# Kernel tuning notes

Hardware: AMD Instinct MI355X
Metric: run time of the kernel (lower is better)

## Reference

```python
import jax, jax.numpy as jnp
import numpy as np

PE_DIM = 40  # pe_dim; gaussian PE scale factor = pe_dim // 2


def _batched_linear(x, wb):
    # x: [B, N, D], wb: [B, D+1, H] (last row is bias)
    return jnp.einsum('bnd,bdh->bnh', x, wb[:, :-1, :]) + wb[:, -1:, :]


def setup_inputs() -> dict:
    key = jax.random.key(0)
    ks = jax.random.split(key, 8)
    B, N = 16, 16384
    H = 256
    pe_out = 3 * PE_DIM  # 120
    s = 0.05  # keep ReLU-chain activations bounded
    return {
        'x': jax.random.normal(ks[0], (B, N, 3), dtype=jnp.float32),
        'wb0': jax.random.normal(ks[1], (B, pe_out + 1, H), dtype=jnp.float32) * s,
        'wb1': jax.random.normal(ks[2], (B, H + 1, H), dtype=jnp.float32) * s,
        'wb2': jax.random.normal(ks[3], (B, H + 1, H), dtype=jnp.float32) * s,
        'wb3': jax.random.normal(ks[4], (B, H + 1, H), dtype=jnp.float32) * s,
        'wb4': jax.random.normal(ks[5], (B, H + 1, H), dtype=jnp.float32) * s,
        'wb_out': jax.random.normal(ks[6], (B, H + 1, 1), dtype=jnp.float32) * s,
        'rand_freqs': jax.random.normal(ks[7], (3 * (PE_DIM // 2), 3), dtype=jnp.float32),  # feat_sigma=1
    }


def reference(x, wb0, wb1, wb2, wb3, wb4, wb_out, rand_freqs):
    # Gaussian positional encoding: k = x . (rand_freqs * pe_dim//2)
    k = jnp.einsum('bnd,fd->bnf', x, rand_freqs * (PE_DIM // 2))  # [B,N,60]
    h = jnp.concatenate([jnp.sin(k), jnp.cos(k)], axis=-1)        # [B,N,120]
    for wb in (wb0, wb1, wb2, wb3, wb4):
        h = jax.nn.relu(_batched_linear(h, wb))
    out = _batched_linear(h, wb_out)  # [B,N,1]
    return out
```

## Files before the change

### kernel.cpp

```cpp
#include <hip/hip_runtime.h>
#include <hip/hip_bf16.h>


#define H 256
#define MT 64
#define PE_NF 60

typedef __attribute__((ext_vector_type(8))) short s16x8;
typedef __attribute__((ext_vector_type(4))) float f32x4;

static __device__ __forceinline__ unsigned short f2bf(float v) {
  unsigned int u = __float_as_uint(v);
  return (unsigned short)((u + 0x7FFFu + ((u >> 16) & 1u)) >> 16);
}
static __device__ __forceinline__ float bf2f(unsigned short u) {
  return __uint_as_float(((unsigned int)u) << 16);
}
static __device__ __forceinline__ int hswz(int row, int chunk) {
  return (chunk & ~7) | ((chunk ^ row) & 7);
}

static __device__ __forceinline__ void bar_raw() {
  asm volatile("s_barrier" ::: "memory");
}
static __device__ __forceinline__ void bar_lgkm() {
  asm volatile("s_waitcnt lgkmcnt(0)\n\ts_barrier" ::: "memory");
}

__global__ __launch_bounds__(256) void prep_weights(
    const float* __restrict__ wb0, const float* __restrict__ wb1,
    const float* __restrict__ wb2, const float* __restrict__ wb3,
    const float* __restrict__ wb4,
    unsigned short* __restrict__ w0p, unsigned short* __restrict__ w14p,
    float* __restrict__ biases) {
  int z = blockIdx.z;
  int li = z >> 4, b = z & 15;
  int k0 = blockIdx.x * 32;
  int n0 = blockIdx.y * 32;
  int Ks;
  const float* src;
  unsigned short* dst;
  if (li == 0) {
    Ks = 120;
    if (k0 >= 128) return;
    src = wb0 + (size_t)b * 121 * H;
    dst = w0p + (size_t)b * 32768;
  } else {
    Ks = 256;
    const float* srcs[4] = {wb1, wb2, wb3, wb4};
    src = srcs[li - 1] + (size_t)b * 257 * H;
    dst = w14p + ((size_t)(li - 1) * 16 + b) * 65536;
  }
  __shared__ float tile[32][33];
  int t = threadIdx.x;
  int tx = t & 31, ty = t >> 5;
#pragma unroll
  for (int i = 0; i < 4; ++i) {
    int k = k0 + ty + i * 8;
    tile[ty + i * 8][tx] = (k < Ks) ? src[(size_t)k * H + n0 + tx] : 0.f;
  }
  if (k0 == 0 && ty == 0)
    biases[((size_t)li * 16 + b) * H + n0 + tx] = src[(size_t)Ks * H + n0 + tx];
  __syncthreads();
  if (t < 128) {
    int nn = t & 31, kg = t >> 5;
    int n = n0 + nn;
    int kt = k0 >> 5;
    union { unsigned short us[8]; s16x8 v; } pk;
#pragma unroll
    for (int j = 0; j < 8; ++j) pk.us[j] = f2bf(tile[kg * 8 + j][nn]);
    *(s16x8*)&dst[(size_t)(kt * 16 + (n >> 4)) * 512 + (kg * 16 + (n & 15)) * 8] = pk.v;
  }
}

template <int NKT, bool LAST>
static __device__ __forceinline__ void mlp_layer(
    const unsigned short* __restrict__ wl, const unsigned short* __restrict__ wln,
    const float* __restrict__ bl, unsigned short* __restrict__ h_s,
    const int rlane, const int kgrp, const int wc, const int l,
    s16x8 (&wf)[2][4]) {
  static_assert((NKT & 1) == 0, "ping-pong parity needs even NKT");
  f32x4 acc[4][4];
#pragma unroll
  for (int ct = 0; ct < 4; ++ct) {
    f32x4 bini = *(const f32x4*)(bl + wc * 64 + ct * 16 + kgrp * 4);
#pragma unroll
    for (int rt = 0; rt < 4; ++rt) acc[rt][ct] = bini;
  }

  const unsigned short* fp = wl + (size_t)(wc * 4) * 512 + l * 8;

  s16x8 af[2][4];
  {
    const int cs = hswz(rlane, kgrp) * 8;
#pragma unroll
    for (int rt = 0; rt < 4; ++rt)
      af[0][rt] = *(const s16x8*)&h_s[(rt * 16 + rlane) * 256 + cs];
  }

#pragma unroll
  for (int kt = 0; kt < NKT; ++kt) {
    if (kt + 1 < NKT) {
#pragma unroll
      for (int c = 0; c < 4; ++c)
        wf[(kt + 1) & 1][c] = *(const s16x8*)(fp + ((kt + 1) * 16 + c) * 512);
      const int cs = hswz(rlane, (kt + 1) * 4 + kgrp) * 8;
#pragma unroll
      for (int rt = 0; rt < 4; ++rt)
        af[(kt + 1) & 1][rt] = *(const s16x8*)&h_s[(rt * 16 + rlane) * 256 + cs];
    } else if (!LAST) {
      const unsigned short* fpn = wln + (size_t)(wc * 4) * 512 + l * 8;
#pragma unroll
      for (int c = 0; c < 4; ++c)
        wf[0][c] = *(const s16x8*)(fpn + c * 512);
    }
    __builtin_amdgcn_s_setprio(1);
#pragma unroll
    for (int rt = 0; rt < 4; ++rt)
#pragma unroll
      for (int ct = 0; ct < 4; ++ct)
        acc[rt][ct] = __builtin_amdgcn_mfma_f32_16x16x32_bf16(
            wf[kt & 1][ct], af[kt & 1][rt], acc[rt][ct], 0, 0, 0);
    __builtin_amdgcn_s_setprio(0);
  }
  bar_raw();

  const int sub = (kgrp & 1) * 4;
  const int cbase = wc * 8 + (kgrp >> 1);
#pragma unroll
  for (int rt = 0; rt < 4; ++rt) {
    const int m = rt * 16 + rlane;
    const int rowb = m * 256;
#pragma unroll
    for (int ct = 0; ct < 4; ++ct) {
      const int cs = hswz(m, cbase + ct * 2);
      float v0 = fmaxf(acc[rt][ct][0], 0.f);
      float v1 = fmaxf(acc[rt][ct][1], 0.f);
      float v2 = fmaxf(acc[rt][ct][2], 0.f);
      float v3 = fmaxf(acc[rt][ct][3], 0.f);
      union { __hip_bfloat162 h2[2]; uint2 u; } pk;
      pk.h2[0] = __float22bfloat162_rn(float2{v0, v1});
      pk.h2[1] = __float22bfloat162_rn(float2{v2, v3});
      *(uint2*)&h_s[rowb + cs * 8 + sub] = pk.u;
    }
  }
  bar_lgkm();
}

__global__ __launch_bounds__(256, 3) void hyponerf_main(
    const float* __restrict__ x, const float* __restrict__ rfreq,
    const float* __restrict__ wbout,
    const unsigned short* __restrict__ w0p, const unsigned short* __restrict__ w14p,
    const float* __restrict__ biases, float* __restrict__ out) {
  __shared__ __align__(16) unsigned short h_s[MT * 256];
  __shared__ float fr_s[PE_NF * 3];
  __shared__ float x_s[MT * 3];
  __shared__ float wout_s[H + 1];

  int bid = blockIdx.x;
  int logical = (bid & 7) * 512 + (bid >> 3);
  int b  = logical >> 8;
  int mt = logical & 255;

  int t = threadIdx.x;
  int wc = t >> 6, l = t & 63;
  int rlane = l & 15;
  int kgrp  = l >> 4;

  const unsigned short* wl0 = w0p + (size_t)b * 32768;
  const unsigned short* wl1 = w14p + (size_t)(0 * 16 + b) * 65536;
  const unsigned short* wl2 = w14p + (size_t)(1 * 16 + b) * 65536;
  const unsigned short* wl3 = w14p + (size_t)(2 * 16 + b) * 65536;
  const unsigned short* wl4 = w14p + (size_t)(3 * 16 + b) * 65536;

  s16x8 wf[2][4];
  {
    const unsigned short* fp0 = wl0 + (size_t)(wc * 4) * 512 + l * 8;
#pragma unroll
    for (int c = 0; c < 4; ++c) wf[0][c] = *(const s16x8*)(fp0 + c * 512);
  }

  const float* xg = x + ((size_t)b * 16384 + (size_t)mt * MT) * 3;
  for (int i = t; i < MT * 3; i += 256) x_s[i] = xg[i];
  for (int i = t; i < PE_NF * 3; i += 256) fr_s[i] = rfreq[i] * 20.0f;
  for (int i = t; i < H + 1; i += 256) wout_s[i] = wbout[(size_t)b * (H + 1) + i];
  bar_lgkm();

  {
    int r = t >> 2;
    int q = t & 3;
    float x0 = x_s[r * 3 + 0], x1 = x_s[r * 3 + 1], x2 = x_s[r * 3 + 2];
    int rowb = r * 256;
#pragma unroll
    for (int cc = 0; cc < 4; ++cc) {
      int ch = q * 4 + cc;
      union { unsigned short us[8]; s16x8 v; } pk;
#pragma unroll
      for (int j = 0; j < 8; ++j) {
        int n = ch * 8 + j;
        float v = 0.f;
        if (n < 60) {
          float kv = x0 * fr_s[n * 3] + x1 * fr_s[n * 3 + 1] + x2 * fr_s[n * 3 + 2];
          v = __sinf(kv);
        } else if (n < 120) {
          int f = n - 60;
          float kv = x0 * fr_s[f * 3] + x1 * fr_s[f * 3 + 1] + x2 * fr_s[f * 3 + 2];
          v = __cosf(kv);
        }
        pk.us[j] = f2bf(v);
      }
      *(s16x8*)&h_s[rowb + hswz(r, ch) * 8] = pk.v;
    }
  }
  bar_lgkm();

  mlp_layer<4, false>(wl0, wl1, biases + (size_t)(0 * 16 + b) * H, h_s,
                      rlane, kgrp, wc, l, wf);
  mlp_layer<8, false>(wl1, wl2, biases + (size_t)(1 * 16 + b) * H, h_s,
                      rlane, kgrp, wc, l, wf);
  mlp_layer<8, false>(wl2, wl3, biases + (size_t)(2 * 16 + b) * H, h_s,
                      rlane, kgrp, wc, l, wf);
  mlp_layer<8, false>(wl3, wl4, biases + (size_t)(3 * 16 + b) * H, h_s,
                      rlane, kgrp, wc, l, wf);
  mlp_layer<8, true >(wl4, wl4, biases + (size_t)(4 * 16 + b) * H, h_s,
                      rlane, kgrp, wc, l, wf);

  {
    int r = t >> 2;
    int q = t & 3;
    int rowb = r * 256;
    float sum = 0.f;
#pragma unroll
    for (int c = 0; c < 8; ++c) {
      int ch = q * 8 + c;
      const s16x8 hv = *(const s16x8*)&h_s[rowb + hswz(r, ch) * 8];
#pragma unroll
      for (int j = 0; j < 8; ++j)
        sum += bf2f((unsigned short)hv[j]) * wout_s[ch * 8 + j];
    }
    sum += __shfl_xor(sum, 1);
    sum += __shfl_xor(sum, 2);
    if (q == 0)
      out[(size_t)b * 16384 + (size_t)mt * MT + r] = sum + wout_s[H];
  }
}

extern "C" void kernel_launch(void* const* d_in, const int* in_sizes, int n_in,
                              void* d_out, int out_size, void* d_ws, size_t ws_size,
                              hipStream_t stream) {
  const float* x     = (const float*)d_in[0];
  const float* wb0   = (const float*)d_in[1];
  const float* wb1   = (const float*)d_in[2];
  const float* wb2   = (const float*)d_in[3];
  const float* wb3   = (const float*)d_in[4];
  const float* wb4   = (const float*)d_in[5];
  const float* wbout = (const float*)d_in[6];
  const float* rfreq = (const float*)d_in[7];
  float* out = (float*)d_out;

  char* ws = (char*)d_ws;
  unsigned short* w0p  = (unsigned short*)ws;
  unsigned short* w14p = (unsigned short*)(ws + (size_t)16 * 32768 * 2);
  float* biases = (float*)(ws + (size_t)16 * 32768 * 2
                              + (size_t)64 * 65536 * 2);

  prep_weights<<<dim3(8, 8, 80), 256, 0, stream>>>(wb0, wb1, wb2, wb3, wb4,
                                                   w0p, w14p, biases);
  hyponerf_main<<<dim3(4096), 256, 0, stream>>>(x, rfreq, wbout, w0p, w14p,
                                                biases, out);
}
```

Baseline: 170.9 us.

## Fuse output projection into last layer epilogue and simplify address arithmetic

The final 256->1 projection is now computed straight from the last layer's fp32 accumulators in registers. Each wave reduces across lanes with shuffles and writes partial sums to a small shared buffer, which replaces the bf16 write-back to shared memory, a barrier and the re-read of h_s. Weight and activation addresses now use precomputed byte pointers and base offsets to cut per-iteration index math. The output projection also consumes unrounded fp32 activations instead of bf16, and the cached output weights add 16 registers per thread, which may pressure occupancy.

```diff
diff --git a/kernel.cpp b/kernel.cpp
--- a/kernel.cpp
+++ b/kernel.cpp
@@ -12,9 +12,6 @@
 static __device__ __forceinline__ unsigned short f2bf(float v) {
   unsigned int u = __float_as_uint(v);
   return (unsigned short)((u + 0x7FFFu + ((u >> 16) & 1u)) >> 16);
-}
-static __device__ __forceinline__ float bf2f(unsigned short u) {
-  return __uint_as_float(((unsigned int)u) << 16);
 }
 static __device__ __forceinline__ int hswz(int row, int chunk) {
   return (chunk & ~7) | ((chunk ^ row) & 7);
@@ -75,10 +72,10 @@
 
 template <int NKT, bool LAST>
 static __device__ __forceinline__ void mlp_layer(
-    const unsigned short* __restrict__ wl, const unsigned short* __restrict__ wln,
-    const float* __restrict__ bl, unsigned short* __restrict__ h_s,
+    const char* fpb, const char* fpn, const float* __restrict__ bl,
+    unsigned short* __restrict__ h_s,
     const int rlane, const int kgrp, const int wc, const int l,
-    s16x8 (&wf)[2][4]) {
+    s16x8 (&wf)[2][4], const float* wout_r, float* psum) {
   static_assert((NKT & 1) == 0, "ping-pong parity needs even NKT");
   f32x4 acc[4][4];
 #pragma unroll
@@ -88,31 +85,31 @@
     for (int rt = 0; rt < 4; ++rt) acc[rt][ct] = bini;
   }
 
-  const unsigned short* fp = wl + (size_t)(wc * 4) * 512 + l * 8;
+  const char* hb = (const char*)h_s;
+  const unsigned be = rlane * 512 + hswz(rlane, kgrp) * 16;
+  const unsigned bo = rlane * 512 + hswz(rlane, 4 + kgrp) * 16;
 
   s16x8 af[2][4];
-  {
-    const int cs = hswz(rlane, kgrp) * 8;
-#pragma unroll
-    for (int rt = 0; rt < 4; ++rt)
-      af[0][rt] = *(const s16x8*)&h_s[(rt * 16 + rlane) * 256 + cs];
-  }
+#pragma unroll
+  for (int rt = 0; rt < 4; ++rt)
+    af[0][rt] = *(const s16x8*)(hb + be + rt * 8192);
 
 #pragma unroll
   for (int kt = 0; kt < NKT; ++kt) {
     if (kt + 1 < NKT) {
+      fpb += 16384;
 #pragma unroll
       for (int c = 0; c < 4; ++c)
-        wf[(kt + 1) & 1][c] = *(const s16x8*)(fp + ((kt + 1) * 16 + c) * 512);
-      const int cs = hswz(rlane, (kt + 1) * 4 + kgrp) * 8;
+        wf[(kt + 1) & 1][c] = *(const s16x8*)(fpb + c * 1024);
+      const unsigned base = ((kt + 1) & 1) ? bo : be;
+      const unsigned off = ((kt + 1) >> 1) * 128;
 #pragma unroll
       for (int rt = 0; rt < 4; ++rt)
-        af[(kt + 1) & 1][rt] = *(const s16x8*)&h_s[(rt * 16 + rlane) * 256 + cs];
+        af[(kt + 1) & 1][rt] = *(const s16x8*)(hb + base + off + rt * 8192);
     } else if (!LAST) {
-      const unsigned short* fpn = wln + (size_t)(wc * 4) * 512 + l * 8;
 #pragma unroll
       for (int c = 0; c < 4; ++c)
-        wf[0][c] = *(const s16x8*)(fpn + c * 512);
+        wf[0][c] = *(const s16x8*)(fpn + c * 1024);
     }
     __builtin_amdgcn_s_setprio(1);
 #pragma unroll
@@ -123,28 +120,49 @@
             wf[kt & 1][ct], af[kt & 1][rt], acc[rt][ct], 0, 0, 0);
     __builtin_amdgcn_s_setprio(0);
   }
-  bar_raw();
-
-  const int sub = (kgrp & 1) * 4;
-  const int cbase = wc * 8 + (kgrp >> 1);
-#pragma unroll
-  for (int rt = 0; rt < 4; ++rt) {
-    const int m = rt * 16 + rlane;
-    const int rowb = m * 256;
-#pragma unroll
-    for (int ct = 0; ct < 4; ++ct) {
-      const int cs = hswz(m, cbase + ct * 2);
-      float v0 = fmaxf(acc[rt][ct][0], 0.f);
-      float v1 = fmaxf(acc[rt][ct][1], 0.f);
-      float v2 = fmaxf(acc[rt][ct][2], 0.f);
-      float v3 = fmaxf(acc[rt][ct][3], 0.f);
-      union { __hip_bfloat162 h2[2]; uint2 u; } pk;
-      pk.h2[0] = __float22bfloat162_rn(float2{v0, v1});
-      pk.h2[1] = __float22bfloat162_rn(float2{v2, v3});
-      *(uint2*)&h_s[rowb + cs * 8 + sub] = pk.u;
-    }
-  }
-  bar_lgkm();
+
+  if constexpr (LAST) {
+    float p[4];
+#pragma unroll
+    for (int rt = 0; rt < 4; ++rt) {
+      float s = 0.f;
+#pragma unroll
+      for (int ct = 0; ct < 4; ++ct)
+#pragma unroll
+        for (int g = 0; g < 4; ++g)
+          s += fmaxf(acc[rt][ct][g], 0.f) * wout_r[ct * 4 + g];
+      s += __shfl_xor(s, 16);
+      s += __shfl_xor(s, 32);
+      p[rt] = s;
+    }
+    if (l < 16) {
+#pragma unroll
+      for (int rt = 0; rt < 4; ++rt)
+        psum[wc * 64 + rt * 16 + l] = p[rt];
+    }
+  } else {
+    bar_raw();
+    const int sub = (kgrp & 1) * 4;
+    const int cbase = wc * 8 + (kgrp >> 1);
+#pragma unroll
+    for (int rt = 0; rt < 4; ++rt) {
+      const int m = rt * 16 + rlane;
+      const int rowb = m * 256;
+#pragma unroll
+      for (int ct = 0; ct < 4; ++ct) {
+        const int cs = hswz(m, cbase + ct * 2);
+        float v0 = fmaxf(acc[rt][ct][0], 0.f);
+        float v1 = fmaxf(acc[rt][ct][1], 0.f);
+        float v2 = fmaxf(acc[rt][ct][2], 0.f);
+        float v3 = fmaxf(acc[rt][ct][3], 0.f);
+        union { __hip_bfloat162 h2[2]; uint2 u; } pk;
+        pk.h2[0] = __float22bfloat162_rn(float2{v0, v1});
+        pk.h2[1] = __float22bfloat162_rn(float2{v2, v3});
+        *(uint2*)&h_s[rowb + cs * 8 + sub] = pk.u;
+      }
+    }
+    bar_lgkm();
+  }
 }
 
 __global__ __launch_bounds__(256, 3) void hyponerf_main(
@@ -155,7 +173,7 @@
   __shared__ __align__(16) unsigned short h_s[MT * 256];
   __shared__ float fr_s[PE_NF * 3];
   __shared__ float x_s[MT * 3];
-  __shared__ float wout_s[H + 1];
+  __shared__ float psum[4 * 64];
 
   int bid = blockIdx.x;
   int logical = (bid & 7) * 512 + (bid >> 3);
@@ -167,23 +185,30 @@
   int rlane = l & 15;
   int kgrp  = l >> 4;
 
-  const unsigned short* wl0 = w0p + (size_t)b * 32768;
-  const unsigned short* wl1 = w14p + (size_t)(0 * 16 + b) * 65536;
-  const unsigned short* wl2 = w14p + (size_t)(1 * 16 + b) * 65536;
-  const unsigned short* wl3 = w14p + (size_t)(2 * 16 + b) * 65536;
-  const unsigned short* wl4 = w14p + (size_t)(3 * 16 + b) * 65536;
+  const size_t lane_off = ((size_t)wc * 4 * 512 + l * 8) * 2;
+  const char* f0 = (const char*)(w0p + (size_t)b * 32768) + lane_off;
+  const char* f1 = (const char*)(w14p + (size_t)(0 * 16 + b) * 65536) + lane_off;
+  const char* f2 = (const char*)(w14p + (size_t)(1 * 16 + b) * 65536) + lane_off;
+  const char* f3 = (const char*)(w14p + (size_t)(2 * 16 + b) * 65536) + lane_off;
+  const char* f4 = (const char*)(w14p + (size_t)(3 * 16 + b) * 65536) + lane_off;
 
   s16x8 wf[2][4];
+#pragma unroll
+  for (int c = 0; c < 4; ++c) wf[0][c] = *(const s16x8*)(f0 + c * 1024);
+
+  float wout_r[16];
   {
-    const unsigned short* fp0 = wl0 + (size_t)(wc * 4) * 512 + l * 8;
-#pragma unroll
-    for (int c = 0; c < 4; ++c) wf[0][c] = *(const s16x8*)(fp0 + c * 512);
-  }
+    const float* wob = wbout + (size_t)b * (H + 1) + wc * 64 + kgrp * 4;
+#pragma unroll
+    for (int ct = 0; ct < 4; ++ct)
+#pragma unroll
+      for (int g = 0; g < 4; ++g) wout_r[ct * 4 + g] = wob[ct * 16 + g];
+  }
+  const float wout_bias = wbout[(size_t)b * (H + 1) + H];
 
   const float* xg = x + ((size_t)b * 16384 + (size_t)mt * MT) * 3;
   for (int i = t; i < MT * 3; i += 256) x_s[i] = xg[i];
   for (int i = t; i < PE_NF * 3; i += 256) fr_s[i] = rfreq[i] * 20.0f;
-  for (int i = t; i < H + 1; i += 256) wout_s[i] = wbout[(size_t)b * (H + 1) + i];
   bar_lgkm();
 
   {
@@ -214,34 +239,22 @@
   }
   bar_lgkm();
 
-  mlp_layer<4, false>(wl0, wl1, biases + (size_t)(0 * 16 + b) * H, h_s,
-                      rlane, kgrp, wc, l, wf);
-  mlp_layer<8, false>(wl1, wl2, biases + (size_t)(1 * 16 + b) * H, h_s,
-                      rlane, kgrp, wc, l, wf);
-  mlp_layer<8, false>(wl2, wl3, biases + (size_t)(2 * 16 + b) * H, h_s,
-                      rlane, kgrp, wc, l, wf);
-  mlp_layer<8, false>(wl3, wl4, biases + (size_t)(3 * 16 + b) * H, h_s,
-                      rlane, kgrp, wc, l, wf);
-  mlp_layer<8, true >(wl4, wl4, biases + (size_t)(4 * 16 + b) * H, h_s,
-                      rlane, kgrp, wc, l, wf);
-
-  {
-    int r = t >> 2;
-    int q = t & 3;
-    int rowb = r * 256;
-    float sum = 0.f;
-#pragma unroll
-    for (int c = 0; c < 8; ++c) {
-      int ch = q * 8 + c;
-      const s16x8 hv = *(const s16x8*)&h_s[rowb + hswz(r, ch) * 8];
-#pragma unroll
-      for (int j = 0; j < 8; ++j)
-        sum += bf2f((unsigned short)hv[j]) * wout_s[ch * 8 + j];
-    }
-    sum += __shfl_xor(sum, 1);
-    sum += __shfl_xor(sum, 2);
-    if (q == 0)
-      out[(size_t)b * 16384 + (size_t)mt * MT + r] = sum + wout_s[H];
+  const float* bb = biases + (size_t)b * H;
+  mlp_layer<4, false>(f0, f1, bb + 0 * 16 * H, h_s, rlane, kgrp, wc, l, wf,
+                      wout_r, psum);
+  mlp_layer<8, false>(f1, f2, bb + 1 * 16 * H, h_s, rlane, kgrp, wc, l, wf,
+                      wout_r, psum);
+  mlp_layer<8, false>(f2, f3, bb + 2 * 16 * H, h_s, rlane, kgrp, wc, l, wf,
+                      wout_r, psum);
+  mlp_layer<8, false>(f3, f4, bb + 3 * 16 * H, h_s, rlane, kgrp, wc, l, wf,
+                      wout_r, psum);
+  mlp_layer<8, true >(f4, f4, bb + 4 * 16 * H, h_s, rlane, kgrp, wc, l, wf,
+                      wout_r, psum);
+
+  bar_lgkm();
+  if (t < MT) {
+    float s = psum[t] + psum[64 + t] + psum[128 + t] + psum[192 + t];
+    out[(size_t)b * 16384 + (size_t)mt * MT + t] = s + wout_bias;
   }
 }
 
```

New measurement: 165.7 us. -3.0%, faster.
